# Optimization experiments

Measured on AMD Instinct MI355X. Metric: run time of the kernel, lower is better.

Reference implementation:

```python
import jax, jax.numpy as jnp
import numpy as np

B, C, H, W = 16, 512, 64, 64
WS = 16            # window size -> N = 256 tokens per window
NH = 16            # num heads, head_dim = 32
HD = C // NH
HID = int((4 * C * 0.5) / 64) * 64   # SwiGLU hidden = 1024
CPB = 512
EPS = 1e-5


def _rel_tables(ws):
    r = np.arange(-(ws - 1), ws, dtype=np.float32)
    tab = np.stack(np.meshgrid(r, r, indexing='ij'), axis=-1)  # (2ws-1,2ws-1,2)
    tab = tab / (ws - 1)
    tab = tab * 8.0
    tab = np.sign(tab) * np.log2(np.abs(tab) + 1.0) / np.log2(8.0)
    # relative position index (N,N)
    coords = np.stack(np.meshgrid(np.arange(ws), np.arange(ws), indexing='ij'))
    cf = coords.reshape(2, -1)
    rel = (cf[:, :, None] - cf[:, None, :]).transpose(1, 2, 0).astype(np.int64)
    rel[:, :, 0] += ws - 1
    rel[:, :, 1] += ws - 1
    rel[:, :, 0] *= 2 * ws - 1
    idx = rel.sum(-1)
    return tab.reshape(-1, 2), idx


def setup_inputs() -> dict:
    key = jax.random.key(0)
    ks = jax.random.split(key, 12)
    s = 0.02
    tab, idx = _rel_tables(WS)
    return {
        'x': jax.random.normal(ks[0], (B, C, H, W), jnp.float32),
        'rel_table': jnp.asarray(tab),
        'norm1_w': jnp.ones((C,), jnp.float32),
        'norm1_b': jnp.zeros((C,), jnp.float32),
        'norm2_w': jnp.ones((C,), jnp.float32),
        'norm2_b': jnp.zeros((C,), jnp.float32),
        'qkv_w': jax.random.normal(ks[1], (C, 3 * C), jnp.float32) * s,
        'proj_w': jax.random.normal(ks[2], (C, C), jnp.float32) * s,
        'cpb_w1': jax.random.normal(ks[3], (2, CPB), jnp.float32) * s,
        'cpb_b1': jnp.zeros((CPB,), jnp.float32),
        'cpb_w2': jax.random.normal(ks[4], (CPB, NH), jnp.float32) * s,
        'fc1_w': jax.random.normal(ks[5], (C, 2 * HID), jnp.float32) * s,
        'fc2_w': jax.random.normal(ks[6], (HID, C), jnp.float32) * s,
        'rel_index': jnp.asarray(idx),
    }


def _ln(x, w, b):
    m = jnp.mean(x, axis=-1, keepdims=True)
    v = jnp.mean(jnp.square(x - m), axis=-1, keepdims=True)
    return (x - m) * jax.lax.rsqrt(v + EPS) * w + b


def reference(x, rel_table, norm1_w, norm1_b, norm2_w, norm2_b, qkv_w, proj_w,
              cpb_w1, cpb_b1, cpb_w2, fc1_w, fc2_w, rel_index):
    ws, nh, hd = WS, NH, HD
    N = ws * ws
    # window partition: (B,C,H,W) -> (B*nW, N, C)
    xw = x.reshape(B, C, H // ws, ws, W // ws, ws)
    xw = xw.transpose(0, 2, 4, 3, 5, 1).reshape(-1, N, C)
    Bw = xw.shape[0]

    # --- window attention ---
    h = _ln(xw, norm1_w, norm1_b)
    qkv = (h @ qkv_w).reshape(Bw, N, 3, nh, hd).transpose(2, 0, 3, 1, 4)
    q, k, v = qkv[0], qkv[1], qkv[2]          # (Bw, nh, N, hd)
    attn = jnp.einsum('bhnd,bhmd->bhnm', q, k) * (hd ** -0.5)
    # Swin-v2 continuous position bias MLP + gather
    bias_tab = jax.nn.relu(rel_table @ cpb_w1 + cpb_b1) @ cpb_w2   # ((2ws-1)^2, nh)
    bias = bias_tab[rel_index]                 # (N, N, nh)
    bias = 16.0 * jax.nn.sigmoid(bias.transpose(2, 0, 1))          # (nh, N, N)
    attn = jax.nn.softmax(attn + bias[None], axis=-1)
    o = jnp.einsum('bhnm,bhmd->bhnd', attn, v)
    o = o.transpose(0, 2, 1, 3).reshape(Bw, N, C) @ proj_w
    xw = xw + o

    # --- SwiGLU MLP ---
    h2 = _ln(xw, norm2_w, norm2_b)
    u = h2 @ fc1_w
    val, gate = jnp.split(u, 2, axis=-1)       # Mlp/SwiGLU: chunk -> silu(gate)*x
    xw = xw + (jax.nn.silu(gate) * val) @ fc2_w

    # window reverse + outer skip
    xr = xw.reshape(B, H // ws, W // ws, ws, ws, C)
    xr = xr.transpose(0, 5, 1, 3, 2, 4).reshape(B, C, H, W)
    return xr + x
```

## Files before the change

kernel.cpp:

```cpp
#include <hip/hip_runtime.h>
#include <hip/hip_bf16.h>

typedef unsigned short u16;
typedef unsigned int u32;
typedef __attribute__((ext_vector_type(8))) u16 u16x8;
typedef __attribute__((ext_vector_type(4))) u16 u16x4;
typedef __attribute__((ext_vector_type(8))) short bf16x8;
typedef __attribute__((ext_vector_type(4))) float f32x4;

__device__ __forceinline__ u16 f2bf(float f) {
  u32 u = __float_as_uint(f);
  u += 0x7fffu + ((u >> 16) & 1u);
  return (u16)(u >> 16);
}
__device__ __forceinline__ float bf2f(u16 h) {
  return __uint_as_float(((u32)h) << 16);
}
__device__ __forceinline__ u16 cvt_bf(float f) {
  __hip_bfloat16 h(f);
  return __builtin_bit_cast(u16, h);
}
__device__ __forceinline__ bf16x8 ld_bf8(const u16* p) {
  return __builtin_bit_cast(bf16x8, *(const u16x8*)p);
}

#if __has_builtin(__builtin_amdgcn_exp2f)
#define EXP2(x) __builtin_amdgcn_exp2f(x)
#else
#define EXP2(x) exp2f(x)
#endif

typedef const void __attribute__((address_space(1)))* gas_t;
typedef void __attribute__((address_space(3)))* las_t;
#define GLOAD_LDS16(gp, lp) __builtin_amdgcn_global_load_lds((gas_t)(gp), (las_t)(lp), 16, 0, 0)

#define QSCALE 0.25503486f
#define BIAS_MUL 23.08312065f

__global__ void wtrans_kernel(const float* __restrict__ in, u16* __restrict__ out, int K, int N) {
  int idx = blockIdx.x * 256 + threadIdx.x;
  if (idx >= K * N) return;
  int n = idx / K, k = idx - n * K;
  out[idx] = f2bf(in[(size_t)k * N + n]);
}

__global__ void wtrans_fc1_kernel(const float* __restrict__ in, u16* __restrict__ out) {
  int idx = blockIdx.x * 256 + threadIdx.x;
  int n = idx >> 9, k = idx & 511;
  int i = ((n >> 5) << 4) | (n & 15);
  int gsel = (n >> 4) & 1;
  out[idx] = f2bf(in[(size_t)k * 2048 + i + gsel * 1024]);
}

__global__ void cpb_kernel(const float* __restrict__ rt, const float* __restrict__ w1,
                           const float* __restrict__ b1, const float* __restrict__ w2,
                           float* __restrict__ tab2) {
  __shared__ float hid[512];
  __shared__ float part[16][17];
  int tix = blockIdx.x;
  int t = threadIdx.x;
  float r0 = rt[tix * 2], r1 = rt[tix * 2 + 1];
  for (int j = t; j < 512; j += 256) {
    float v = r0 * w1[j] + r1 * w1[512 + j] + b1[j];
    hid[j] = v > 0.f ? v : 0.f;
  }
  __syncthreads();
  int hh = t & 15, seg = t >> 4;
  float acc = 0.f;
  for (int j = seg * 32; j < seg * 32 + 32; ++j) acc += hid[j] * w2[j * 16 + hh];
  part[seg][hh] = acc;
  __syncthreads();
  if (t < 16) {
    float s = 0.f;
    for (int g = 0; g < 16; ++g) s += part[g][t];
    tab2[t * 961 + tix] = BIAS_MUL / (1.f + __expf(-s)) - 23.0f;
  }
}

__global__ __launch_bounds__(256, 4) void ln1_kernel(
    const float* __restrict__ x, const float* __restrict__ w, const float* __restrict__ b,
    u16* __restrict__ hbuf, u16* __restrict__ xwbuf) {
  __shared__ u16 tile[512 * 33];
  __shared__ float red[2][8][32];
  __shared__ float meanv[32], rstdv[32];
  int bi = blockIdx.x;
  int bimg = bi >> 7, rest = bi & 127, hrow = rest >> 1, half = rest & 1;
  int t = threadIdx.x, p = t & 31, g = t >> 5;
  const float* xr = x + (size_t)bimg * 512 * 4096 + (size_t)hrow * 64 + half * 32;
  float s = 0.f, s2 = 0.f;
  for (int i = 0; i < 64; ++i) {
    int c = g * 64 + i;
    float v = xr[(size_t)c * 4096 + p];
    tile[c * 33 + p] = f2bf(v);
    s += v; s2 += v * v;
  }
  red[0][g][p] = s; red[1][g][p] = s2;
  __syncthreads();
  if (t < 32) {
    float ss = 0.f, qq = 0.f;
    for (int gg = 0; gg < 8; ++gg) { ss += red[0][gg][t]; qq += red[1][gg][t]; }
    float mu = ss * (1.f / 512.f);
    float var = qq * (1.f / 512.f) - mu * mu;
    meanv[t] = mu;
    rstdv[t] = rsqrtf(var + 1e-5f);
  }
  __syncthreads();
  int c0 = t * 2;
  float w0 = w[c0], w1v = w[c0 + 1], b0 = b[c0], b1v = b[c0 + 1];
  int hy = hrow >> 4, iy = hrow & 15;
  for (int pp = 0; pp < 32; ++pp) {
    int pixel = half * 32 + pp;
    int wx = pixel >> 4, ix = pixel & 15;
    int widx = bimg * 16 + hy * 4 + wx;
    size_t basep = ((size_t)widx * 256 + iy * 16 + ix) * 512;
    u16 rb0 = tile[c0 * 33 + pp], rb1 = tile[(c0 + 1) * 33 + pp];
    float mu = meanv[pp], rs = rstdv[pp];
    float v0 = bf2f(rb0), v1 = bf2f(rb1);
    *(u32*)(xwbuf + basep + c0) = (u32)rb0 | ((u32)rb1 << 16);
    u16 h0 = f2bf((v0 - mu) * rs * w0 + b0);
    u16 h1 = f2bf((v1 - mu) * rs * w1v + b1v);
    *(u32*)(hbuf + basep + c0) = (u32)h0 | ((u32)h1 << 16);
  }
}

template <int EPI>
__global__ __launch_bounds__(256, 4) void gemm_bt(
    const u16* __restrict__ A, const u16* __restrict__ Bt,
    u16* __restrict__ out, const u16* __restrict__ res,
    u16* __restrict__ q_o, u16* __restrict__ k_o, u16* __restrict__ v_o,
    const float* __restrict__ xg, float* __restrict__ outf,
    int M, int N, int K) {
  __shared__ u16 As[128 * 64];
  __shared__ u16 Bs[128 * 64];
  const int t = threadIdx.x, l = t & 63, wv = t >> 6;
  const int nbx = N >> 7;
  const int wg = (int)blockIdx.x;
  const int xcd = wg & 7, c = wg >> 3;
  const int cm = c / nbx;
  const int m0 = (xcd * 64 + cm) * 128, n0 = (c - cm * nbx) * 128;
  const int wr = wv >> 1, wc = wv & 1;
  const int lr = l & 15, lk = l >> 4;
  f32x4 acc[4][4] = {};
  for (int kt = 0; kt < K; kt += 64) {
#pragma unroll
    for (int j = 0; j < 4; ++j) {
      int qi = j * 256 + t;
      int r = qi >> 3, c8 = (qi & 7) * 8;
      GLOAD_LDS16(A + (size_t)(m0 + r) * K + kt + c8, As + (size_t)(j * 256 + wv * 64) * 8);
    }
#pragma unroll
    for (int j = 0; j < 4; ++j) {
      int qi = j * 256 + t;
      int r = qi >> 3, c8 = (qi & 7) * 8;
      GLOAD_LDS16(Bt + (size_t)(n0 + r) * K + kt + c8, Bs + (size_t)(j * 256 + wv * 64) * 8);
    }
    __syncthreads();
#pragma unroll
    for (int ks = 0; ks < 2; ++ks) {
      bf16x8 a[4], bb[4];
#pragma unroll
      for (int mf = 0; mf < 4; ++mf)
        a[mf] = ld_bf8(As + (wr * 64 + mf * 16 + lr) * 64 + ks * 32 + lk * 8);
#pragma unroll
      for (int nf = 0; nf < 4; ++nf)
        bb[nf] = ld_bf8(Bs + (wc * 64 + nf * 16 + lr) * 64 + ks * 32 + lk * 8);
#pragma unroll
      for (int mf = 0; mf < 4; ++mf)
#pragma unroll
        for (int nf = 0; nf < 4; ++nf)
          acc[mf][nf] = __builtin_amdgcn_mfma_f32_16x16x32_bf16(a[mf], bb[nf], acc[mf][nf], 0, 0, 0);
    }
    __syncthreads();
  }
#pragma unroll
  for (int mf = 0; mf < 4; ++mf) {
    int rbase = m0 + wr * 64 + mf * 16 + lk * 4;
    if constexpr (EPI == 3) {
#pragma unroll
      for (int nf = 0; nf < 4; nf += 2) {
        int colv = n0 + wc * 64 + nf * 16 + lr;
        int i = ((colv >> 5) << 4) | (colv & 15);
#pragma unroll
        for (int jj = 0; jj < 4; ++jj) {
          int row = rbase + jj;
          float val = acc[mf][nf][jj], gate = acc[mf][nf + 1][jj];
          float sil = gate / (1.f + __expf(-gate));
          out[(size_t)row * 1024 + i] = f2bf(sil * val);
        }
      }
    } else if constexpr (EPI == 4) {
      int widx = rbase >> 8, iy = (rbase >> 4) & 15, ix0 = rbase & 15;
      int bimg = widx >> 4, hy = (widx >> 2) & 3, wx = widx & 3;
#pragma unroll
      for (int nf = 0; nf < 4; ++nf) {
        int col = n0 + wc * 64 + nf * 16 + lr;
        size_t obase = (((size_t)(bimg * 512 + col) * 64) + hy * 16 + iy) * 64 + wx * 16 + ix0;
        const float* xp = xg + obase;
        float* op = outf + obase;
#pragma unroll
        for (int jj = 0; jj < 4; ++jj)
          op[jj] = acc[mf][nf][jj] + bf2f(res[(size_t)(rbase + jj) * 512 + col]) + xp[jj];
      }
    } else {
#pragma unroll
      for (int nf = 0; nf < 4; ++nf) {
        int col = n0 + wc * 64 + nf * 16 + lr;
#pragma unroll
        for (int jj = 0; jj < 4; ++jj) {
          int row = rbase + jj;
          float v = acc[mf][nf][jj];
          if constexpr (EPI == 0) {
            out[(size_t)row * N + col] = f2bf(v);
          } else if constexpr (EPI == 1) {
            out[(size_t)row * N + col] = f2bf(v + bf2f(res[(size_t)row * N + col]));
          } else if constexpr (EPI == 2) {
            int which = col >> 9, rem = col & 511;
            int hh = rem >> 5, dd = rem & 31;
            size_t dst = (((size_t)(row >> 8) * 16 + hh) * 256 + (size_t)(row & 255)) * 32 + dd;
            u16* po = which == 0 ? q_o : (which == 1 ? k_o : v_o);
            float sc = which == 0 ? QSCALE : 1.f;
            po[dst] = f2bf(v * sc);
          }
        }
      }
    }
  }
}

__global__ __launch_bounds__(256, 4) void attn_kernel(
    const u16* __restrict__ qb, const u16* __restrict__ kb, const u16* __restrict__ vb,
    const float* __restrict__ tab2, u16* __restrict__ ob) {
  __shared__ u16 vt[32 * 72];
  __shared__ float tabh4[31 * 32 * 4];
  __shared__ u16 pl[4][16 * 76];
  const int w = blockIdx.x, h = blockIdx.y;
  const int t = threadIdx.x, l = t & 63, wid = t >> 6;
  const size_t base = (size_t)(w * 16 + h) * 256 * 32;
  const u16* qg = qb + base;
  const u16* kg = kb + base;
  const u16* vg = vb + base;
  const float* th = tab2 + h * 961;
  for (int i = t; i < 992; i += 256) {
    int dy = i >> 5, dx = i & 31;
#pragma unroll
    for (int r = 0; r < 4; ++r) {
      int dxr = dx + r;
      tabh4[i * 4 + r] = (dxr <= 30) ? th[dy * 31 + dxr] : 0.f;
    }
  }
  const int q4 = l >> 4, c0 = l & 15;
  const int dx0 = q4 * 4 - c0 + 15;
  bf16x8 qa[4];
#pragma unroll
  for (int mf = 0; mf < 4; ++mf)
    qa[mf] = ld_bf8(qg + (wid * 64 + mf * 16 + c0) * 32 + q4 * 8);
  f32x4 oacc[4][2] = {};
  float psum[4][4] = {};
  for (int ct = 0; ct < 4; ++ct) {
    {
      int r = t & 63, j = t >> 6;
      u16x8 dv = *(const u16x8*)(vg + (ct * 64 + r) * 32 + j * 8);
#pragma unroll
      for (int e = 0; e < 8; ++e) vt[(j * 8 + e) * 72 + r] = dv[e];
    }
    __syncthreads();
    bf16x8 bfr[4];
#pragma unroll
    for (int nf = 0; nf < 4; ++nf)
      bfr[nf] = ld_bf8(kg + (ct * 64 + nf * 16 + c0) * 32 + q4 * 8);
    bf16x8 vfr[2][2];
#pragma unroll
    for (int df = 0; df < 2; ++df)
#pragma unroll
      for (int ks2 = 0; ks2 < 2; ++ks2)
        vfr[df][ks2] = ld_bf8(vt + (df * 16 + c0) * 72 + ks2 * 32 + q4 * 8);
#pragma unroll
    for (int mf = 0; mf < 4; ++mf) {
      const int dyb = wid * 4 + mf - ct * 4 + 15;
      f32x4 sacc[4];
#pragma unroll
      for (int nf = 0; nf < 4; ++nf)
        sacc[nf] = *(const f32x4*)&tabh4[((dyb - nf) * 32 + dx0) * 4];
      __builtin_amdgcn_s_setprio(1);
#pragma unroll
      for (int nf = 0; nf < 4; ++nf)
        sacc[nf] = __builtin_amdgcn_mfma_f32_16x16x32_bf16(qa[mf], bfr[nf], sacc[nf], 0, 0, 0);
      __builtin_amdgcn_s_setprio(0);
#pragma unroll
      for (int nf = 0; nf < 4; ++nf) {
#pragma unroll
        for (int jj = 0; jj < 4; ++jj) {
          float p = EXP2(sacc[nf][jj]);
          psum[mf][jj] += p;
          pl[wid][(q4 * 4 + jj) * 76 + nf * 16 + c0] = cvt_bf(p);
        }
      }
      __builtin_amdgcn_s_setprio(1);
#pragma unroll
      for (int ks2 = 0; ks2 < 2; ++ks2) {
        bf16x8 pa = ld_bf8(&pl[wid][c0 * 76 + ks2 * 32 + q4 * 8]);
        oacc[mf][0] = __builtin_amdgcn_mfma_f32_16x16x32_bf16(pa, vfr[0][ks2], oacc[mf][0], 0, 0, 0);
        oacc[mf][1] = __builtin_amdgcn_mfma_f32_16x16x32_bf16(pa, vfr[1][ks2], oacc[mf][1], 0, 0, 0);
      }
      __builtin_amdgcn_s_setprio(0);
    }
    __syncthreads();
  }
#pragma unroll
  for (int mf = 0; mf < 4; ++mf) {
#pragma unroll
    for (int jj = 0; jj < 4; ++jj) {
      float s = psum[mf][jj];
      s += __shfl_xor(s, 1);
      s += __shfl_xor(s, 2);
      s += __shfl_xor(s, 4);
      s += __shfl_xor(s, 8);
      float inv = 1.f / s;
      int row = wid * 64 + mf * 16 + q4 * 4 + jj;
      size_t obase = ((size_t)w * 256 + row) * 512 + h * 32;
      ob[obase + c0] = f2bf(oacc[mf][0][jj] * inv);
      ob[obase + 16 + c0] = f2bf(oacc[mf][1][jj] * inv);
    }
  }
}

__global__ __launch_bounds__(256, 4) void ln2_kernel(const u16* __restrict__ r1,
    const float* __restrict__ w, const float* __restrict__ b, u16* __restrict__ h2) {
  int t = threadIdx.x, l = t & 63, wid = t >> 6;
  size_t token = (size_t)blockIdx.x * 4 + wid;
  const u16* rp = r1 + token * 512 + l * 8;
  u16x8 raw = *(const u16x8*)rp;
  float v[8]; float s = 0.f, s2 = 0.f;
#pragma unroll
  for (int i = 0; i < 8; ++i) { v[i] = bf2f(raw[i]); s += v[i]; s2 += v[i] * v[i]; }
#pragma unroll
  for (int m = 1; m < 64; m <<= 1) { s += __shfl_xor(s, m); s2 += __shfl_xor(s2, m); }
  float mu = s * (1.f / 512.f);
  float var = s2 * (1.f / 512.f) - mu * mu;
  float rs = rsqrtf(var + 1e-5f);
  u16x8 o;
#pragma unroll
  for (int i = 0; i < 8; ++i) {
    int c = l * 8 + i;
    o[i] = f2bf((v[i] - mu) * rs * w[c] + b[c]);
  }
  *(u16x8*)(h2 + token * 512 + l * 8) = o;
}

extern "C" void kernel_launch(void* const* d_in, const int* in_sizes, int n_in,
                              void* d_out, int out_size, void* d_ws, size_t ws_size,
                              hipStream_t stream) {
  (void)in_sizes; (void)n_in; (void)out_size; (void)ws_size;
  const float* x = (const float*)d_in[0];
  const float* rel_table = (const float*)d_in[1];
  const float* n1w = (const float*)d_in[2];
  const float* n1b = (const float*)d_in[3];
  const float* n2w = (const float*)d_in[4];
  const float* n2b = (const float*)d_in[5];
  const float* qkv_w = (const float*)d_in[6];
  const float* proj_w = (const float*)d_in[7];
  const float* cpb_w1 = (const float*)d_in[8];
  const float* cpb_b1 = (const float*)d_in[9];
  const float* cpb_w2 = (const float*)d_in[10];
  const float* fc1_w = (const float*)d_in[11];
  const float* fc2_w = (const float*)d_in[12];
  float* outp = (float*)d_out;
  char* ws = (char*)d_ws;

  u16* wq = (u16*)(ws + 0);
  u16* wp = (u16*)(ws + 1572864);
  u16* w1 = (u16*)(ws + 2097152);
  u16* w2 = (u16*)(ws + 4194304);
  float* tab2 = (float*)(ws + 5242880);
  const size_t RB = 67108864;
  u16* R0 = (u16*)(ws + 8388608);
  u16* R1 = (u16*)(ws + 8388608 + RB);
  u16* R2 = (u16*)(ws + 8388608 + 2 * RB);
  u16* R3 = (u16*)(ws + 8388608 + 3 * RB);
  u16* R4 = (u16*)(ws + 8388608 + 4 * RB);
  u16* R5 = (u16*)(ws + 8388608 + 5 * RB);

  wtrans_kernel<<<3072, 256, 0, stream>>>(qkv_w, wq, 512, 1536);
  wtrans_kernel<<<1024, 256, 0, stream>>>(proj_w, wp, 512, 512);
  wtrans_fc1_kernel<<<4096, 256, 0, stream>>>(fc1_w, w1);
  wtrans_kernel<<<2048, 256, 0, stream>>>(fc2_w, w2, 1024, 512);
  cpb_kernel<<<961, 256, 0, stream>>>(rel_table, cpb_w1, cpb_b1, cpb_w2, tab2);
  ln1_kernel<<<2048, 256, 0, stream>>>(x, n1w, n1b, R2, R0);
  gemm_bt<2><<<6144, 256, 0, stream>>>(R2, wq, nullptr, nullptr,
                                       R3, R4, R5, nullptr, nullptr, 65536, 1536, 512);
  attn_kernel<<<dim3(256, 16), 256, 0, stream>>>(R3, R4, R5, tab2, R2);
  gemm_bt<1><<<2048, 256, 0, stream>>>(R2, wp, R1, R0,
                                       nullptr, nullptr, nullptr, nullptr, nullptr, 65536, 512, 512);
  ln2_kernel<<<16384, 256, 0, stream>>>(R1, n2w, n2b, R3);
  gemm_bt<3><<<8192, 256, 0, stream>>>(R3, w1, R4, nullptr,
                                       nullptr, nullptr, nullptr, nullptr, nullptr, 65536, 2048, 512);
  gemm_bt<4><<<2048, 256, 0, stream>>>(R4, w2, nullptr, R1,
                                       nullptr, nullptr, nullptr, x, outp, 65536, 512, 1024);
}
```

Measured before the change: 759.3 us.

## Add 256x256 double-buffered GEMM kernel for QKV and FC1 projections

```diff
diff --git a/kernel.cpp b/kernel.cpp
--- a/kernel.cpp
+++ b/kernel.cpp
@@ -127,7 +127,6 @@
 __global__ __launch_bounds__(256, 4) void gemm_bt(
     const u16* __restrict__ A, const u16* __restrict__ Bt,
     u16* __restrict__ out, const u16* __restrict__ res,
-    u16* __restrict__ q_o, u16* __restrict__ k_o, u16* __restrict__ v_o,
     const float* __restrict__ xg, float* __restrict__ outf,
     int M, int N, int K) {
   __shared__ u16 As[128 * 64];
@@ -175,6 +174,144 @@
 #pragma unroll
   for (int mf = 0; mf < 4; ++mf) {
     int rbase = m0 + wr * 64 + mf * 16 + lk * 4;
+    if constexpr (EPI == 4) {
+      int widx = rbase >> 8, iy = (rbase >> 4) & 15, ix0 = rbase & 15;
+      int bimg = widx >> 4, hy = (widx >> 2) & 3, wx = widx & 3;
+#pragma unroll
+      for (int nf = 0; nf < 4; ++nf) {
+        int col = n0 + wc * 64 + nf * 16 + lr;
+        size_t obase = (((size_t)(bimg * 512 + col) * 64) + hy * 16 + iy) * 64 + wx * 16 + ix0;
+        const float* xp = xg + obase;
+        float* op = outf + obase;
+#pragma unroll
+        for (int jj = 0; jj < 4; ++jj)
+          op[jj] = acc[mf][nf][jj] + bf2f(res[(size_t)(rbase + jj) * 512 + col]) + xp[jj];
+      }
+    } else {
+#pragma unroll
+      for (int nf = 0; nf < 4; ++nf) {
+        int col = n0 + wc * 64 + nf * 16 + lr;
+#pragma unroll
+        for (int jj = 0; jj < 4; ++jj) {
+          int row = rbase + jj;
+          out[(size_t)row * N + col] = f2bf(acc[mf][nf][jj] + bf2f(res[(size_t)row * N + col]));
+        }
+      }
+    }
+  }
+}
+
+template <int EPI>
+__global__ __launch_bounds__(512, 2) void gemm8(
+    const u16* __restrict__ A, const u16* __restrict__ Bt,
+    u16* __restrict__ out,
+    u16* __restrict__ q_o, u16* __restrict__ k_o, u16* __restrict__ v_o,
+    int N, int K) {
+  __shared__ u16 As[2][256 * 64];
+  __shared__ u16 Bs[2][256 * 64];
+  const int t = threadIdx.x;
+  const int l = t & 63;
+  const int wid = t >> 6;
+  const int wr = wid >> 2, wc = wid & 3;
+  const int lr = l & 15, lk = l >> 4;
+  const int nbx = N >> 8;
+  const int wg = (int)blockIdx.x;
+  const int xcd = wg & 7, c = wg >> 3;
+  const int cm = c / nbx;
+  const int m0 = (xcd * 32 + cm) * 256;
+  const int n0 = (c - cm * nbx) * 256;
+  const int swz = lr & 7;
+
+  auto stage = [&](int b, int kt) {
+#pragma unroll
+    for (int j = 0; j < 4; ++j) {
+      int seg = j * 512 + t;
+      int row = seg >> 3, s = seg & 7;
+      int col8 = (s ^ (row & 7)) << 3;
+      GLOAD_LDS16(A + (size_t)(m0 + row) * K + kt + col8, &As[b][seg * 8]);
+    }
+#pragma unroll
+    for (int j = 0; j < 4; ++j) {
+      int seg = j * 512 + t;
+      int row = seg >> 3, s = seg & 7;
+      int col8 = (s ^ (row & 7)) << 3;
+      GLOAD_LDS16(Bt + (size_t)(n0 + row) * K + kt + col8, &Bs[b][seg * 8]);
+    }
+  };
+
+  f32x4 acc[8][4] = {};
+  const int nt = K >> 6;
+  stage(0, 0);
+  for (int tt = 0; tt < nt; ++tt) {
+    if (tt + 1 < nt) {
+      stage((tt + 1) & 1, (tt + 1) * 64);
+      asm volatile("s_waitcnt vmcnt(8)" ::: "memory");
+    } else {
+      asm volatile("s_waitcnt vmcnt(0)" ::: "memory");
+    }
+    __builtin_amdgcn_s_barrier();
+    const u16* as = &As[tt & 1][0];
+    const u16* bs = &Bs[tt & 1][0];
+    bf16x8 af[4], bf[4];
+#pragma unroll
+    for (int mf = 0; mf < 4; ++mf)
+      af[mf] = ld_bf8(as + (wr * 128 + mf * 16 + lr) * 64 + ((lk ^ swz) << 3));
+#pragma unroll
+    for (int nf = 0; nf < 4; ++nf)
+      bf[nf] = ld_bf8(bs + (wc * 64 + nf * 16 + lr) * 64 + ((lk ^ swz) << 3));
+    __builtin_amdgcn_s_barrier();
+    __builtin_amdgcn_s_setprio(1);
+#pragma unroll
+    for (int mf = 0; mf < 4; ++mf)
+#pragma unroll
+      for (int nf = 0; nf < 4; ++nf)
+        acc[mf][nf] = __builtin_amdgcn_mfma_f32_16x16x32_bf16(af[mf], bf[nf], acc[mf][nf], 0, 0, 0);
+    __builtin_amdgcn_s_setprio(0);
+    __builtin_amdgcn_s_barrier();
+    bf16x8 ag[4];
+#pragma unroll
+    for (int mf = 0; mf < 4; ++mf)
+      ag[mf] = ld_bf8(as + (wr * 128 + (mf + 4) * 16 + lr) * 64 + ((lk ^ swz) << 3));
+    __builtin_amdgcn_s_barrier();
+    __builtin_amdgcn_s_setprio(1);
+#pragma unroll
+    for (int mf = 0; mf < 4; ++mf)
+#pragma unroll
+      for (int nf = 0; nf < 4; ++nf)
+        acc[mf + 4][nf] = __builtin_amdgcn_mfma_f32_16x16x32_bf16(ag[mf], bf[nf], acc[mf + 4][nf], 0, 0, 0);
+    __builtin_amdgcn_s_setprio(0);
+    __builtin_amdgcn_s_barrier();
+#pragma unroll
+    for (int mf = 0; mf < 4; ++mf)
+      af[mf] = ld_bf8(as + (wr * 128 + mf * 16 + lr) * 64 + (((4 | lk) ^ swz) << 3));
+#pragma unroll
+    for (int nf = 0; nf < 4; ++nf)
+      bf[nf] = ld_bf8(bs + (wc * 64 + nf * 16 + lr) * 64 + (((4 | lk) ^ swz) << 3));
+    __builtin_amdgcn_s_barrier();
+    __builtin_amdgcn_s_setprio(1);
+#pragma unroll
+    for (int mf = 0; mf < 4; ++mf)
+#pragma unroll
+      for (int nf = 0; nf < 4; ++nf)
+        acc[mf][nf] = __builtin_amdgcn_mfma_f32_16x16x32_bf16(af[mf], bf[nf], acc[mf][nf], 0, 0, 0);
+    __builtin_amdgcn_s_setprio(0);
+    __builtin_amdgcn_s_barrier();
+#pragma unroll
+    for (int mf = 0; mf < 4; ++mf)
+      ag[mf] = ld_bf8(as + (wr * 128 + (mf + 4) * 16 + lr) * 64 + (((4 | lk) ^ swz) << 3));
+    __builtin_amdgcn_s_barrier();
+    __builtin_amdgcn_s_setprio(1);
+#pragma unroll
+    for (int mf = 0; mf < 4; ++mf)
+#pragma unroll
+      for (int nf = 0; nf < 4; ++nf)
+        acc[mf + 4][nf] = __builtin_amdgcn_mfma_f32_16x16x32_bf16(ag[mf], bf[nf], acc[mf + 4][nf], 0, 0, 0);
+    __builtin_amdgcn_s_setprio(0);
+    __builtin_amdgcn_s_barrier();
+  }
+#pragma unroll
+  for (int mf = 0; mf < 8; ++mf) {
+    int rbase = m0 + wr * 128 + mf * 16 + lk * 4;
     if constexpr (EPI == 3) {
 #pragma unroll
       for (int nf = 0; nf < 4; nf += 2) {
@@ -188,39 +325,19 @@
           out[(size_t)row * 1024 + i] = f2bf(sil * val);
         }
       }
-    } else if constexpr (EPI == 4) {
-      int widx = rbase >> 8, iy = (rbase >> 4) & 15, ix0 = rbase & 15;
-      int bimg = widx >> 4, hy = (widx >> 2) & 3, wx = widx & 3;
+    } else {
 #pragma unroll
       for (int nf = 0; nf < 4; ++nf) {
         int col = n0 + wc * 64 + nf * 16 + lr;
-        size_t obase = (((size_t)(bimg * 512 + col) * 64) + hy * 16 + iy) * 64 + wx * 16 + ix0;
-        const float* xp = xg + obase;
-        float* op = outf + obase;
-#pragma unroll
-        for (int jj = 0; jj < 4; ++jj)
-          op[jj] = acc[mf][nf][jj] + bf2f(res[(size_t)(rbase + jj) * 512 + col]) + xp[jj];
-      }
-    } else {
-#pragma unroll
-      for (int nf = 0; nf < 4; ++nf) {
-        int col = n0 + wc * 64 + nf * 16 + lr;
+        int which = col >> 9, rem = col & 511;
+        int hh = rem >> 5, dd = rem & 31;
+        u16* po = which == 0 ? q_o : (which == 1 ? k_o : v_o);
+        float sc = which == 0 ? QSCALE : 1.f;
 #pragma unroll
         for (int jj = 0; jj < 4; ++jj) {
           int row = rbase + jj;
-          float v = acc[mf][nf][jj];
-          if constexpr (EPI == 0) {
-            out[(size_t)row * N + col] = f2bf(v);
-          } else if constexpr (EPI == 1) {
-            out[(size_t)row * N + col] = f2bf(v + bf2f(res[(size_t)row * N + col]));
-          } else if constexpr (EPI == 2) {
-            int which = col >> 9, rem = col & 511;
-            int hh = rem >> 5, dd = rem & 31;
-            size_t dst = (((size_t)(row >> 8) * 16 + hh) * 256 + (size_t)(row & 255)) * 32 + dd;
-            u16* po = which == 0 ? q_o : (which == 1 ? k_o : v_o);
-            float sc = which == 0 ? QSCALE : 1.f;
-            po[dst] = f2bf(v * sc);
-          }
+          size_t dst = (((size_t)(row >> 8) * 16 + hh) * 256 + (size_t)(row & 255)) * 32 + dd;
+          po[dst] = f2bf(acc[mf][nf][jj] * sc);
         }
       }
     }
@@ -386,14 +503,12 @@
   wtrans_kernel<<<2048, 256, 0, stream>>>(fc2_w, w2, 1024, 512);
   cpb_kernel<<<961, 256, 0, stream>>>(rel_table, cpb_w1, cpb_b1, cpb_w2, tab2);
   ln1_kernel<<<2048, 256, 0, stream>>>(x, n1w, n1b, R2, R0);
-  gemm_bt<2><<<6144, 256, 0, stream>>>(R2, wq, nullptr, nullptr,
-                                       R3, R4, R5, nullptr, nullptr, 65536, 1536, 512);
+  gemm8<2><<<1536, 512, 0, stream>>>(R2, wq, nullptr, R3, R4, R5, 1536, 512);
   attn_kernel<<<dim3(256, 16), 256, 0, stream>>>(R3, R4, R5, tab2, R2);
   gemm_bt<1><<<2048, 256, 0, stream>>>(R2, wp, R1, R0,
-                                       nullptr, nullptr, nullptr, nullptr, nullptr, 65536, 512, 512);
+                                       nullptr, nullptr, 65536, 512, 512);
   ln2_kernel<<<16384, 256, 0, stream>>>(R1, n2w, n2b, R3);
-  gemm_bt<3><<<8192, 256, 0, stream>>>(R3, w1, R4, nullptr,
-                                       nullptr, nullptr, nullptr, nullptr, nullptr, 65536, 2048, 512);
+  gemm8<3><<<2048, 512, 0, stream>>>(R3, w1, R4, nullptr, nullptr, nullptr, 2048, 512);
   gemm_bt<4><<<2048, 256, 0, stream>>>(R4, w2, nullptr, R1,
-                                       nullptr, nullptr, nullptr, x, outp, 65536, 512, 1024);
-}
+                                       x, outp, 65536, 512, 1024);
+}
```

Result: slower. 809.9 us (+6.7%).

## Drop xw residual buffer and QKV scatter; attention reads packed QKV rows

Applied to the files above, without the earlier changes.

```diff
diff --git a/kernel.cpp b/kernel.cpp
--- a/kernel.cpp
+++ b/kernel.cpp
@@ -42,6 +42,13 @@
   if (idx >= K * N) return;
   int n = idx / K, k = idx - n * K;
   out[idx] = f2bf(in[(size_t)k * N + n]);
+}
+
+__global__ void wtrans_qkv_kernel(const float* __restrict__ in, u16* __restrict__ out) {
+  int idx = blockIdx.x * 256 + threadIdx.x;
+  int n = idx >> 9, k = idx & 511;
+  float s = n < 512 ? QSCALE : 1.f;
+  out[idx] = f2bf(in[(size_t)k * 1536 + n] * s);
 }
 
 __global__ void wtrans_fc1_kernel(const float* __restrict__ in, u16* __restrict__ out) {
@@ -79,7 +86,7 @@
 
 __global__ __launch_bounds__(256, 4) void ln1_kernel(
     const float* __restrict__ x, const float* __restrict__ w, const float* __restrict__ b,
-    u16* __restrict__ hbuf, u16* __restrict__ xwbuf) {
+    u16* __restrict__ hbuf) {
   __shared__ u16 tile[512 * 33];
   __shared__ float red[2][8][32];
   __shared__ float meanv[32], rstdv[32];
@@ -116,7 +123,6 @@
     u16 rb0 = tile[c0 * 33 + pp], rb1 = tile[(c0 + 1) * 33 + pp];
     float mu = meanv[pp], rs = rstdv[pp];
     float v0 = bf2f(rb0), v1 = bf2f(rb1);
-    *(u32*)(xwbuf + basep + c0) = (u32)rb0 | ((u32)rb1 << 16);
     u16 h0 = f2bf((v0 - mu) * rs * w0 + b0);
     u16 h1 = f2bf((v1 - mu) * rs * w1v + b1v);
     *(u32*)(hbuf + basep + c0) = (u32)h0 | ((u32)h1 << 16);
@@ -127,7 +133,6 @@
 __global__ __launch_bounds__(256, 4) void gemm_bt(
     const u16* __restrict__ A, const u16* __restrict__ Bt,
     u16* __restrict__ out, const u16* __restrict__ res,
-    u16* __restrict__ q_o, u16* __restrict__ k_o, u16* __restrict__ v_o,
     const float* __restrict__ xg, float* __restrict__ outf,
     int M, int N, int K) {
   __shared__ u16 As[128 * 64];
@@ -188,7 +193,7 @@
           out[(size_t)row * 1024 + i] = f2bf(sil * val);
         }
       }
-    } else if constexpr (EPI == 4) {
+    } else if constexpr (EPI == 4 || EPI == 5) {
       int widx = rbase >> 8, iy = (rbase >> 4) & 15, ix0 = rbase & 15;
       int bimg = widx >> 4, hy = (widx >> 2) & 3, wx = widx & 3;
 #pragma unroll
@@ -196,49 +201,39 @@
         int col = n0 + wc * 64 + nf * 16 + lr;
         size_t obase = (((size_t)(bimg * 512 + col) * 64) + hy * 16 + iy) * 64 + wx * 16 + ix0;
         const float* xp = xg + obase;
-        float* op = outf + obase;
-#pragma unroll
-        for (int jj = 0; jj < 4; ++jj)
-          op[jj] = acc[mf][nf][jj] + bf2f(res[(size_t)(rbase + jj) * 512 + col]) + xp[jj];
+        if constexpr (EPI == 4) {
+          float* op = outf + obase;
+#pragma unroll
+          for (int jj = 0; jj < 4; ++jj)
+            op[jj] = acc[mf][nf][jj] + bf2f(res[(size_t)(rbase + jj) * 512 + col]) + xp[jj];
+        } else {
+#pragma unroll
+          for (int jj = 0; jj < 4; ++jj)
+            out[(size_t)(rbase + jj) * 512 + col] = f2bf(acc[mf][nf][jj] + xp[jj]);
+        }
       }
     } else {
 #pragma unroll
       for (int nf = 0; nf < 4; ++nf) {
         int col = n0 + wc * 64 + nf * 16 + lr;
 #pragma unroll
-        for (int jj = 0; jj < 4; ++jj) {
-          int row = rbase + jj;
-          float v = acc[mf][nf][jj];
-          if constexpr (EPI == 0) {
-            out[(size_t)row * N + col] = f2bf(v);
-          } else if constexpr (EPI == 1) {
-            out[(size_t)row * N + col] = f2bf(v + bf2f(res[(size_t)row * N + col]));
-          } else if constexpr (EPI == 2) {
-            int which = col >> 9, rem = col & 511;
-            int hh = rem >> 5, dd = rem & 31;
-            size_t dst = (((size_t)(row >> 8) * 16 + hh) * 256 + (size_t)(row & 255)) * 32 + dd;
-            u16* po = which == 0 ? q_o : (which == 1 ? k_o : v_o);
-            float sc = which == 0 ? QSCALE : 1.f;
-            po[dst] = f2bf(v * sc);
-          }
-        }
+        for (int jj = 0; jj < 4; ++jj)
+          out[(size_t)(rbase + jj) * N + col] = f2bf(acc[mf][nf][jj]);
       }
     }
   }
 }
 
 __global__ __launch_bounds__(256, 4) void attn_kernel(
-    const u16* __restrict__ qb, const u16* __restrict__ kb, const u16* __restrict__ vb,
-    const float* __restrict__ tab2, u16* __restrict__ ob) {
+    const u16* __restrict__ qkv, const float* __restrict__ tab2, u16* __restrict__ ob) {
   __shared__ u16 vt[32 * 72];
   __shared__ float tabh4[31 * 32 * 4];
   __shared__ u16 pl[4][16 * 76];
-  const int w = blockIdx.x, h = blockIdx.y;
+  const int h = blockIdx.x, w = blockIdx.y;
   const int t = threadIdx.x, l = t & 63, wid = t >> 6;
-  const size_t base = (size_t)(w * 16 + h) * 256 * 32;
-  const u16* qg = qb + base;
-  const u16* kg = kb + base;
-  const u16* vg = vb + base;
+  const u16* qg = qkv + (size_t)(w * 256) * 1536 + h * 32;
+  const u16* kg = qg + 512;
+  const u16* vg = qg + 1024;
   const float* th = tab2 + h * 961;
   for (int i = t; i < 992; i += 256) {
     int dy = i >> 5, dx = i & 31;
@@ -253,13 +248,13 @@
   bf16x8 qa[4];
 #pragma unroll
   for (int mf = 0; mf < 4; ++mf)
-    qa[mf] = ld_bf8(qg + (wid * 64 + mf * 16 + c0) * 32 + q4 * 8);
+    qa[mf] = ld_bf8(qg + (size_t)(wid * 64 + mf * 16 + c0) * 1536 + q4 * 8);
   f32x4 oacc[4][2] = {};
   float psum[4][4] = {};
   for (int ct = 0; ct < 4; ++ct) {
     {
       int r = t & 63, j = t >> 6;
-      u16x8 dv = *(const u16x8*)(vg + (ct * 64 + r) * 32 + j * 8);
+      u16x8 dv = *(const u16x8*)(vg + (size_t)(ct * 64 + r) * 1536 + j * 8);
 #pragma unroll
       for (int e = 0; e < 8; ++e) vt[(j * 8 + e) * 72 + r] = dv[e];
     }
@@ -267,7 +262,7 @@
     bf16x8 bfr[4];
 #pragma unroll
     for (int nf = 0; nf < 4; ++nf)
-      bfr[nf] = ld_bf8(kg + (ct * 64 + nf * 16 + c0) * 32 + q4 * 8);
+      bfr[nf] = ld_bf8(kg + (size_t)(ct * 64 + nf * 16 + c0) * 1536 + q4 * 8);
     bf16x8 vfr[2][2];
 #pragma unroll
     for (int df = 0; df < 2; ++df)
@@ -373,27 +368,25 @@
   u16* w2 = (u16*)(ws + 4194304);
   float* tab2 = (float*)(ws + 5242880);
   const size_t RB = 67108864;
-  u16* R0 = (u16*)(ws + 8388608);
   u16* R1 = (u16*)(ws + 8388608 + RB);
   u16* R2 = (u16*)(ws + 8388608 + 2 * RB);
   u16* R3 = (u16*)(ws + 8388608 + 3 * RB);
   u16* R4 = (u16*)(ws + 8388608 + 4 * RB);
-  u16* R5 = (u16*)(ws + 8388608 + 5 * RB);
-
-  wtrans_kernel<<<3072, 256, 0, stream>>>(qkv_w, wq, 512, 1536);
+
+  wtrans_qkv_kernel<<<3072, 256, 0, stream>>>(qkv_w, wq);
   wtrans_kernel<<<1024, 256, 0, stream>>>(proj_w, wp, 512, 512);
   wtrans_fc1_kernel<<<4096, 256, 0, stream>>>(fc1_w, w1);
   wtrans_kernel<<<2048, 256, 0, stream>>>(fc2_w, w2, 1024, 512);
   cpb_kernel<<<961, 256, 0, stream>>>(rel_table, cpb_w1, cpb_b1, cpb_w2, tab2);
-  ln1_kernel<<<2048, 256, 0, stream>>>(x, n1w, n1b, R2, R0);
-  gemm_bt<2><<<6144, 256, 0, stream>>>(R2, wq, nullptr, nullptr,
-                                       R3, R4, R5, nullptr, nullptr, 65536, 1536, 512);
-  attn_kernel<<<dim3(256, 16), 256, 0, stream>>>(R3, R4, R5, tab2, R2);
-  gemm_bt<1><<<2048, 256, 0, stream>>>(R2, wp, R1, R0,
-                                       nullptr, nullptr, nullptr, nullptr, nullptr, 65536, 512, 512);
+  ln1_kernel<<<2048, 256, 0, stream>>>(x, n1w, n1b, R2);
+  gemm_bt<0><<<6144, 256, 0, stream>>>(R2, wq, R3, nullptr,
+                                       nullptr, nullptr, 65536, 1536, 512);
+  attn_kernel<<<dim3(16, 256), 256, 0, stream>>>(R3, tab2, R2);
+  gemm_bt<5><<<2048, 256, 0, stream>>>(R2, wp, R1, nullptr,
+                                       x, nullptr, 65536, 512, 512);
   ln2_kernel<<<16384, 256, 0, stream>>>(R1, n2w, n2b, R3);
   gemm_bt<3><<<8192, 256, 0, stream>>>(R3, w1, R4, nullptr,
-                                       nullptr, nullptr, nullptr, nullptr, nullptr, 65536, 2048, 512);
+                                       nullptr, nullptr, 65536, 2048, 512);
   gemm_bt<4><<<2048, 256, 0, stream>>>(R4, w2, nullptr, R1,
-                                       nullptr, nullptr, nullptr, x, outp, 65536, 512, 1024);
-}
+                                       x, outp, 65536, 512, 1024);
+}
```

Result: no change. 746.7 us (-1.7%).
